# Kernel optimization log

Measured on AMD Instinct MI355X. Metric: run time of the kernel, lower is better.

## Reference

```python
import jax, jax.numpy as jnp
import numpy as np

N = 4096          # n_nodes == batch_size (GFN operates on dense [N,N] adjacency)
E = 65536         # edges per view (avg degree 16)
D = [512, 256, 128]
HV = [128, 64]    # hidden_size_v
HM = [64, 32]     # hidden_size


def _xavier(key, shape):
    fan_in, fan_out = shape[0], shape[1]
    lim = np.sqrt(6.0 / (fan_in + fan_out))
    return jax.random.uniform(key, shape, jnp.float32, -lim, lim)


def setup_inputs() -> dict:
    key = jax.random.key(0)
    ks = jax.random.split(key, 40)
    inp = {}
    inp['data1'] = jax.random.normal(ks[0], (N, D[0]), jnp.float32)
    inp['data2'] = jax.random.normal(ks[1], (N, D[1]), jnp.float32)
    inp['data3'] = jax.random.normal(ks[2], (N, D[2]), jnp.float32)
    # graphs: random edge lists + matching dense adjacency (g.ndata['adj'])
    for v, k_ in zip((1, 2, 3), (ks[3], ks[4], ks[5])):
        ka, kb = jax.random.split(k_)
        src = jax.random.randint(ka, (E,), 0, N, jnp.int32)
        dst = jax.random.randint(kb, (E,), 0, N, jnp.int32)
        adj = np.zeros((N, N), np.float32)
        adj[np.asarray(src), np.asarray(dst)] = 1.0
        inp[f'src{v}'] = src
        inp[f'dst{v}'] = dst
        inp[f'adj{v}'] = jnp.asarray(adj)
    # per-view GraphConv weights (DGL GraphConv: weight [in,out], bias [out])
    dims = {1: [D[0]] + HV, 2: [D[1]] + HV, 3: [D[2]] + HV}
    ki = 6
    for v in (1, 2, 3):
        for l in range(len(HV)):
            inp[f'w{v}_{l}'] = _xavier(ks[ki], (dims[v][l], dims[v][l + 1])); ki += 1
            inp[f'b{v}_{l}'] = jnp.zeros((dims[v][l + 1],), jnp.float32)
    # consensus GraphConv stack
    mdims = [HV[-1]] + HM
    for l in range(len(HM)):
        inp[f'wm_{l}'] = _xavier(ks[ki], (mdims[l], mdims[l + 1])); ki += 1
        inp[f'bm_{l}'] = jnp.zeros((mdims[l + 1],), jnp.float32)
    # FeatureFusion weights [HV[-1], HV[-1]]
    inp['fw1'] = _xavier(ks[ki], (HV[-1], HV[-1])); ki += 1
    inp['fw2'] = _xavier(ks[ki], (HV[-1], HV[-1])); ki += 1
    inp['fw3'] = _xavier(ks[ki], (HV[-1], HV[-1])); ki += 1
    # GFN: Linear(N, N//2) -> ReLU -> Linear(N//2, N); torch Linear weight [out,in]
    H = N // 2
    inp['gfn_w1'] = _xavier(ks[ki], (H, N)); ki += 1
    inp['gfn_b1'] = jnp.zeros((H,), jnp.float32)
    inp['gfn_w2'] = _xavier(ks[ki], (N, H)); ki += 1
    inp['gfn_b2'] = jnp.zeros((N,), jnp.float32)
    return inp


def _gconv(src, dst, x, W, b):
    ones = jnp.ones((src.shape[0],), x.dtype)
    deg_out = jnp.clip(jax.ops.segment_sum(ones, src, num_segments=N), 1.0)
    deg_in = jnp.clip(jax.ops.segment_sum(ones, dst, num_segments=N), 1.0)
    h = (x * jax.lax.rsqrt(deg_out)[:, None]) @ W  # diag norms commute with W
    agg = jax.ops.segment_sum(h[src], dst, num_segments=N)
    return agg * jax.lax.rsqrt(deg_in)[:, None] + b


def _dense_gconv(A, x, W, b):
    # same math on a dense (multigraph-count) adjacency; A[src,dst] counts edges
    deg_out = jnp.clip(A.sum(axis=1), 1.0)
    deg_in = jnp.clip(A.sum(axis=0), 1.0)
    h = (x * jax.lax.rsqrt(deg_out)[:, None]) @ W
    agg = A.T @ h
    return agg * jax.lax.rsqrt(deg_in)[:, None] + b


def reference(data1, data2, data3, src1, dst1, src2, dst2, src3, dst3,
              adj1, adj2, adj3,
              w1_0, b1_0, w1_1, b1_1, w2_0, b2_0, w2_1, b2_1,
              w3_0, b3_0, w3_1, b3_1, wm_0, bm_0, wm_1, bm_1,
              fw1, fw2, fw3, gfn_w1, gfn_b1, gfn_w2, gfn_b2):
    # per-view encoder stacks (relu on all but last layer)
    f1 = jax.nn.relu(_gconv(src1, dst1, data1, w1_0, b1_0))
    f1 = _gconv(src1, dst1, f1, w1_1, b1_1)
    f2 = jax.nn.relu(_gconv(src2, dst2, data2, w2_0, b2_0))
    f2 = _gconv(src2, dst2, f2, w2_1, b2_1)
    f3 = jax.nn.relu(_gconv(src3, dst3, data3, w3_0, b3_0))
    f3 = _gconv(src3, dst3, f3, w3_1, b3_1)
    # FeatureFusion (dropout treated as eval/identity): softmax then relu
    z = f1 @ fw1 + f2 @ fw2 + f3 @ fw3
    z = jax.nn.relu(jax.nn.softmax(z, axis=1))
    # consensus graph: GFN on summed dense adjacency
    adjin = adj1 + adj2 + adj3
    adj_r = jax.nn.relu(adjin @ gfn_w1.T + gfn_b1) @ gfn_w2.T + gfn_b2
    adj_p = jnp.round(jnp.clip(adj_r, 0.0, 1.0) + 0.1)
    # dgl.from_scipy on (adj_p + adj_p.T) keeps edge per nonzero; add_self_loop
    # adds one extra self edge per node -> multigraph edge counts = struct + I
    A = ((adj_p + adj_p.T) != 0).astype(jnp.float32) + jnp.eye(N, dtype=jnp.float32)
    A = jax.lax.stop_gradient(A)  # graph built from detached adj_p
    feat = jax.nn.relu(_dense_gconv(A, z, wm_0, bm_0))
    feat = _dense_gconv(A, feat, wm_1, bm_1)
    # InnerProductDecoder with identity activation (same for every view)
    adj_rec = feat @ feat.T
    return adj_r, adj_rec, feat
```

## Files before the change

kernel.cpp:

```cpp
#include <hip/hip_runtime.h>


#define N_ 4096
#define E_ 65536
#define CSR_STRIDE 73732

typedef __attribute__((ext_vector_type(8))) short short8;
typedef __attribute__((ext_vector_type(4))) float f32x4;

__device__ __forceinline__ float bf2f(unsigned short u) {
  union { unsigned int i; float f; } v; v.i = ((unsigned int)u) << 16; return v.f;
}
__device__ __forceinline__ unsigned short f2bf(float f) {
  union { float f; unsigned int i; } v; v.f = f;
  return (unsigned short)((v.i + 0x7fffu + ((v.i >> 16) & 1u)) >> 16);
}

__global__ void k_edges(const int* __restrict__ s1, const int* __restrict__ d1,
                        const int* __restrict__ s2, const int* __restrict__ d2,
                        const int* __restrict__ s3, const int* __restrict__ d3,
                        float* __restrict__ wd, unsigned* __restrict__ bmp) {
  int v = blockIdx.x >> 8;
  int e = (blockIdx.x & 255) * 256 + threadIdx.x;
  const int* sv = v == 0 ? s1 : (v == 1 ? s2 : s3);
  const int* dv = v == 0 ? d1 : (v == 1 ? d2 : d3);
  int s = sv[e], d = dv[e];
  atomicAdd(&wd[v * 8192 + s], 1.f);
  atomicAdd(&wd[v * 8192 + 4096 + d], 1.f);
  unsigned idx = (unsigned)s * 4096u + (unsigned)d;
  atomicOr(&bmp[v * 524288 + (idx >> 5)], 1u << (idx & 31));
}

__global__ void k_prep(const unsigned* __restrict__ bmp, ushort* __restrict__ adjin,
                       const float4* __restrict__ g1, const float4* __restrict__ g2,
                       ushort* __restrict__ w1h, ushort* __restrict__ w1l,
                       ushort* __restrict__ w2h, ushort* __restrict__ w2l) {
  int i = blockIdx.x * 256 + threadIdx.x;
  if (i < 2097152) {
    int w = i >> 2, sh = (i & 3) << 3;
    unsigned a = bmp[w] >> sh, b = bmp[524288 + w] >> sh, c = bmp[1048576 + w] >> sh;
    short8 o;
#pragma unroll
    for (int k = 0; k < 8; ++k) {
      int cnt = ((a >> k) & 1) + ((b >> k) & 1) + ((c >> k) & 1);
      o[k] = (short)f2bf((float)cnt);
    }
    *(short8*)(adjin + (size_t)i * 8) = o;
  } else {
    int i2 = i - 2097152;
    int hf = i2 >= 2097152;
    int j = i2 & 2097151;
    float4 x = hf ? g2[j] : g1[j];
    ushort* ph = hf ? w2h : w1h;
    ushort* pl = hf ? w2l : w1l;
    ushort4 h, l;
    h.x = f2bf(x.x); l.x = f2bf(x.x - bf2f(h.x));
    h.y = f2bf(x.y); l.y = f2bf(x.y - bf2f(h.y));
    h.z = f2bf(x.z); l.z = f2bf(x.z - bf2f(h.z));
    h.w = f2bf(x.w); l.w = f2bf(x.w - bf2f(h.w));
    *(ushort4*)(ph + (size_t)j * 4) = h;
    *(ushort4*)(pl + (size_t)j * 4) = l;
  }
}

__global__ void k_scan7(float* __restrict__ wd, int* __restrict__ csr) {
  int b = blockIdx.x, t = threadIdx.x;
  if (b < 3) {
    float* di = wd + b * 8192 + 4096;
    int* ptr = csr + b * CSR_STRIDE;
    int* cur = ptr + 4100;
    __shared__ int part[256];
    int local[16];
    float cnt[16];
    int s = 0;
#pragma unroll
    for (int i = 0; i < 16; ++i) { cnt[i] = di[t * 16 + i]; local[i] = s; s += (int)cnt[i]; }
    part[t] = s;
    __syncthreads();
    for (int o = 1; o < 256; o <<= 1) {
      int x = (t >= o) ? part[t - o] : 0;
      __syncthreads();
      part[t] += x;
      __syncthreads();
    }
    int base = (t > 0) ? part[t - 1] : 0;
#pragma unroll
    for (int i = 0; i < 16; ++i) {
      ptr[t * 16 + i] = base + local[i];
      cur[t * 16 + i] = 0;
      di[t * 16 + i] = 1.f / sqrtf(fmaxf(cnt[i], 1.f));
    }
    if (t == 255) ptr[4096] = part[255];
  } else {
    int off = (b == 3) ? 0 : (b == 4) ? 8192 : (b == 5) ? 16384 : 24576;
#pragma unroll
    for (int i = 0; i < 16; ++i) {
      int idx = off + t * 16 + i;
      wd[idx] = 1.f / sqrtf(fmaxf(wd[idx], 1.f));
    }
  }
}

__global__ void k_fill(const int* __restrict__ s1, const int* __restrict__ d1,
                       const int* __restrict__ s2, const int* __restrict__ d2,
                       const int* __restrict__ s3, const int* __restrict__ d3,
                       int* __restrict__ csr) {
  int v = blockIdx.x >> 8;
  int e = (blockIdx.x & 255) * 256 + threadIdx.x;
  const int* sv = v == 0 ? s1 : (v == 1 ? s2 : s3);
  const int* dv = v == 0 ? d1 : (v == 1 ? d2 : d3);
  int* ptr = csr + v * CSR_STRIDE;
  int* cur = ptr + 4100;
  int* cidx = cur + 4096;
  int d = dv[e];
  int pos = ptr[d] + atomicAdd(&cur[d], 1);
  cidx[pos] = sv[e];
}

template<int C, int RELU>
__global__ void k_agg(const float* __restrict__ h, const int* __restrict__ csrv,
                      const float* __restrict__ rs, const float* __restrict__ bias,
                      float* __restrict__ out, int os, int oo) {
  const int* ptr = csrv;
  const int* cidx = csrv + 4100 + 4096;
  int wave = threadIdx.x >> 6, lane = threadIdx.x & 63;
  int dst, col;
  if (C == 128) { dst = (blockIdx.x << 1) + (wave >> 1); col = ((wave & 1) << 6) + lane; }
  else          { dst = (blockIdx.x << 2) + wave;        col = lane; }
  int e0 = ptr[dst], e1 = ptr[dst + 1];
  float acc = 0.f;
  for (int e = e0; e < e1; ++e) acc += h[(size_t)cidx[e] * C + col];
  float v = acc * rs[dst] + bias[col];
  if (RELU) v = fmaxf(v, 0.f);
  out[(size_t)dst * os + oo + col] = v;
}

__global__ void k_softmax(const float* __restrict__ zp, float* __restrict__ z) {
  int row = blockIdx.x * 4 + (threadIdx.x >> 6);
  int lane = threadIdx.x & 63;
  float v = zp[row * 64 + lane];
  float m = v;
  for (int o = 32; o; o >>= 1) m = fmaxf(m, __shfl_xor(m, o, 64));
  float e = expf(v - m);
  float s = e;
  for (int o = 32; o; o >>= 1) s += __shfl_xor(s, o, 64);
  z[row * 64 + lane] = e / s;
}

__global__ void k_buildA(const float* __restrict__ adjr, ushort* __restrict__ Ab,
                         float* __restrict__ degA) {
  int bi = blockIdx.y, bj = blockIdx.x;
  if (bi > bj) return;
  __shared__ float t2[64][65];
  __shared__ ushort at[64][65];
  __shared__ float cs[64];
  int t = threadIdx.x, w = t >> 6, lane = t & 63;
#pragma unroll
  for (int i = 0; i < 16; ++i) {
    int idx = t + i * 256, r = idx >> 6, c = idx & 63;
    t2[r][c] = adjr[(size_t)(bj * 64 + r) * N_ + bi * 64 + c];
  }
  if (t < 64) cs[t] = 0.f;
  __syncthreads();
  float colp = 0.f;
  for (int rr = 0; rr < 16; ++rr) {
    int r = w * 16 + rr;
    int gi = bi * 64 + r, gj = bj * 64 + lane;
    float p1 = rintf(fminf(fmaxf(adjr[(size_t)gi * N_ + gj], 0.f), 1.f) + 0.1f);
    float p2 = rintf(fminf(fmaxf(t2[lane][r], 0.f), 1.f) + 0.1f);
    float a = ((p1 + p2) != 0.f ? 1.f : 0.f) + (gi == gj ? 1.f : 0.f);
    ushort ab = f2bf(a);
    Ab[(size_t)gi * N_ + gj] = ab;
    at[lane][r] = ab;
    colp += a;
    float s = a;
    for (int o = 32; o; o >>= 1) s += __shfl_xor(s, o, 64);
    if (lane == 0) atomicAdd(&degA[gi], s);
  }
  if (bi < bj) {
    atomicAdd(&cs[lane], colp);
    __syncthreads();
#pragma unroll
    for (int i = 0; i < 16; ++i) {
      int idx = t + i * 256, r = idx >> 6, c = idx & 63;
      Ab[(size_t)(bj * 64 + r) * N_ + bi * 64 + c] = at[r][c];
    }
    if (t < 64) atomicAdd(&degA[bj * 64 + t], cs[t]);
  }
}

template<int BN, int TM, int RS>
__global__ __launch_bounds__(256) void k_gemm(
    const float* __restrict__ Ap, int lda, const float* __restrict__ B, int ldb,
    float* __restrict__ C, int ldc, int K, const float* __restrict__ rs) {
  __shared__ float As[64][33];
  __shared__ float Bs[32][BN];
  const int t = threadIdx.x;
  const int bm = blockIdx.x << 6;
  const int bn = blockIdx.y * BN;
  const int cg = t % (BN / 4), rg = t / (BN / 4);
  float av[TM][4];
#pragma unroll
  for (int i = 0; i < TM; ++i)
#pragma unroll
    for (int j = 0; j < 4; ++j) av[i][j] = 0.f;
  for (int k0 = 0; k0 < K; k0 += 32) {
    __syncthreads();
#pragma unroll
    for (int i = 0; i < 8; ++i) {
      int idx = t + (i << 8), r = idx >> 5, c = idx & 31;
      As[r][c] = Ap[(size_t)(bm + r) * lda + k0 + c];
    }
#pragma unroll
    for (int i = 0; i < (BN >> 3); ++i) {
      int idx = t + (i << 8), r = idx / BN, c = idx % BN;
      Bs[r][c] = B[(size_t)(k0 + r) * ldb + bn + c];
    }
    __syncthreads();
#pragma unroll
    for (int k = 0; k < 32; ++k) {
      float b0 = Bs[k][(cg << 2) + 0], b1 = Bs[k][(cg << 2) + 1];
      float b2 = Bs[k][(cg << 2) + 2], b3 = Bs[k][(cg << 2) + 3];
#pragma unroll
      for (int i = 0; i < TM; ++i) {
        float a = As[rg * TM + i][k];
        av[i][0] = fmaf(a, b0, av[i][0]);
        av[i][1] = fmaf(a, b1, av[i][1]);
        av[i][2] = fmaf(a, b2, av[i][2]);
        av[i][3] = fmaf(a, b3, av[i][3]);
      }
    }
  }
#pragma unroll
  for (int i = 0; i < TM; ++i) {
    int gm = bm + rg * TM + i;
    float s = RS ? rs[gm] : 1.f;
#pragma unroll
    for (int j = 0; j < 4; ++j)
      C[(size_t)gm * ldc + bn + (cg << 2) + j] = av[i][j] * s;
  }
}

__global__ __launch_bounds__(256) void k_fuse(
    const float* __restrict__ Ap, const float* __restrict__ F1,
    const float* __restrict__ F2, const float* __restrict__ F3,
    float* __restrict__ C) {
  __shared__ float As[64][33];
  __shared__ float Bs[32][32];
  const int t = threadIdx.x;
  const int bm = blockIdx.x << 6;
  const int bn = blockIdx.y * 32;
  const int cg = t % 8, rg = t / 8;
  float av[2][4];
#pragma unroll
  for (int i = 0; i < 2; ++i)
#pragma unroll
    for (int j = 0; j < 4; ++j) av[i][j] = 0.f;
  for (int k0 = 0; k0 < 192; k0 += 32) {
    __syncthreads();
#pragma unroll
    for (int i = 0; i < 8; ++i) {
      int idx = t + (i << 8), r = idx >> 5, c = idx & 31;
      As[r][c] = Ap[(size_t)(bm + r) * 192 + k0 + c];
    }
#pragma unroll
    for (int i = 0; i < 4; ++i) {
      int idx = t + (i << 8), r = idx >> 5, c = idx & 31;
      int gr = k0 + r;
      const float* Bp = gr < 64 ? F1 : (gr < 128 ? F2 : F3);
      Bs[r][c] = Bp[(gr & 63) * 64 + bn + c];
    }
    __syncthreads();
#pragma unroll
    for (int k = 0; k < 32; ++k) {
      float b0 = Bs[k][(cg << 2) + 0], b1 = Bs[k][(cg << 2) + 1];
      float b2 = Bs[k][(cg << 2) + 2], b3 = Bs[k][(cg << 2) + 3];
#pragma unroll
      for (int i = 0; i < 2; ++i) {
        float a = As[rg * 2 + i][k];
        av[i][0] = fmaf(a, b0, av[i][0]);
        av[i][1] = fmaf(a, b1, av[i][1]);
        av[i][2] = fmaf(a, b2, av[i][2]);
        av[i][3] = fmaf(a, b3, av[i][3]);
      }
    }
  }
#pragma unroll
  for (int i = 0; i < 2; ++i)
#pragma unroll
    for (int j = 0; j < 4; ++j)
      C[(size_t)(bm + rg * 2 + i) * 64 + bn + (cg << 2) + j] = av[i][j];
}

template<int C>
__global__ void k_tsplit(const float* __restrict__ in, ushort* __restrict__ hTh,
                         ushort* __restrict__ hTl) {
  __shared__ float tl[64][C + 1];
  int t = threadIdx.x;
  int m0 = blockIdx.x * 64;
#pragma unroll
  for (int i = 0; i < (C >> 2); ++i) {
    int idx = t + (i << 8), r = idx / C, c = idx % C;
    tl[r][c] = in[(size_t)(m0 + r) * C + c];
  }
  __syncthreads();
#pragma unroll
  for (int i = 0; i < (C >> 2); ++i) {
    int idx = t + (i << 8), c = idx >> 6, mm = idx & 63;
    float v = tl[mm][c];
    ushort hh = f2bf(v);
    hTh[(size_t)c * N_ + m0 + mm] = hh;
    hTl[(size_t)c * N_ + m0 + mm] = f2bf(v - bf2f(hh));
  }
}

template<int BN>
__global__ __launch_bounds__(256) void k_aggm(
    const ushort* __restrict__ Ab, const ushort* __restrict__ hTh,
    const ushort* __restrict__ hTl, float* __restrict__ part) {
  constexpr int NF = BN / 16;
  constexpr int BR = BN / 32;
  __shared__ __align__(16) ushort lA[8192];
  __shared__ __align__(16) ushort lBh[BN * 64];
  __shared__ __align__(16) ushort lBl[BN * 64];
  const int t = threadIdx.x, lane = t & 63, wave = t >> 6;
  const int bm = blockIdx.x << 7;
  const int kb = blockIdx.y << 9;
  const int hi = lane >> 4, r16 = lane & 15, rx = r16 & 7;
  const int srow = t >> 3, sslot = t & 7;

  f32x4 acc[2][NF];
#pragma unroll
  for (int i = 0; i < 2; ++i)
#pragma unroll
    for (int j = 0; j < NF; ++j)
#pragma unroll
      for (int r = 0; r < 4; ++r) acc[i][j][r] = 0.f;

  short8 sA[4], sBh[BR], sBl[BR];
#define ALOAD(KT)                                                                     \
  {                                                                                   \
    _Pragma("unroll") for (int i = 0; i < 4; ++i) {                                   \
      int row = (i << 5) + srow;                                                      \
      sA[i] = *(const short8*)(Ab + (size_t)(bm + row) * 4096 + kb + (KT) + (sslot << 3)); \
    }                                                                                 \
    _Pragma("unroll") for (int i = 0; i < BR; ++i) {                                  \
      int row = (i << 5) + srow;                                                      \
      sBh[i] = *(const short8*)(hTh + (size_t)row * 4096 + kb + (KT) + (sslot << 3)); \
      sBl[i] = *(const short8*)(hTl + (size_t)row * 4096 + kb + (KT) + (sslot << 3)); \
    }                                                                                 \
  }
  ALOAD(0);
  for (int kt = 0; kt < 512; kt += 64) {
    __syncthreads();
#pragma unroll
    for (int i = 0; i < 4; ++i) {
      int row = (i << 5) + srow;
      *(short8*)(&lA[row * 64 + ((sslot ^ (row & 7)) << 3)]) = sA[i];
    }
#pragma unroll
    for (int i = 0; i < BR; ++i) {
      int row = (i << 5) + srow;
      *(short8*)(&lBh[row * 64 + ((sslot ^ (row & 7)) << 3)]) = sBh[i];
      *(short8*)(&lBl[row * 64 + ((sslot ^ (row & 7)) << 3)]) = sBl[i];
    }
    __syncthreads();
    if (kt + 64 < 512) ALOAD(kt + 64);
#pragma unroll
    for (int k0 = 0; k0 < 2; ++k0) {
      const int soff = (((k0 << 2) + hi) ^ rx) << 3;
      short8 af[2], bh[NF], bl[NF];
#pragma unroll
      for (int mi = 0; mi < 2; ++mi) {
        int row = wave * 32 + mi * 16 + r16;
        af[mi] = *(const short8*)(&lA[row * 64 + soff]);
      }
#pragma unroll
      for (int ni = 0; ni < NF; ++ni) {
        int row = ni * 16 + r16;
        bh[ni] = *(const short8*)(&lBh[row * 64 + soff]);
        bl[ni] = *(const short8*)(&lBl[row * 64 + soff]);
      }
#pragma unroll
      for (int mi = 0; mi < 2; ++mi)
#pragma unroll
        for (int ni = 0; ni < NF; ++ni) {
          acc[mi][ni] = __builtin_amdgcn_mfma_f32_16x16x32_bf16(af[mi], bh[ni], acc[mi][ni], 0, 0, 0);
          acc[mi][ni] = __builtin_amdgcn_mfma_f32_16x16x32_bf16(af[mi], bl[ni], acc[mi][ni], 0, 0, 0);
        }
    }
  }
#pragma unroll
  for (int mi = 0; mi < 2; ++mi)
#pragma unroll
    for (int ni = 0; ni < NF; ++ni)
#pragma unroll
      for (int r2 = 0; r2 < 4; ++r2) {
        int gm = bm + wave * 32 + mi * 16 + (hi << 2) + r2;
        int gn = ni * 16 + r16;
        part[((size_t)blockIdx.y * 4096 + gm) * BN + gn] = acc[mi][ni][r2];
      }
#undef ALOAD
}

template<int C, int RELU, int WFT>
__global__ void k_fincons(const float* __restrict__ part, const float* __restrict__ rs,
                          const float* __restrict__ bias, float* __restrict__ out,
                          float* __restrict__ featT) {
  int i = blockIdx.x * 256 + threadIdx.x;
  int m = i / C, c = i % C;
  float s = 0.f;
#pragma unroll
  for (int z = 0; z < 8; ++z) s += part[((size_t)z * 4096 + m) * C + c];
  float v = s * rs[m] + bias[c];
  if (RELU) v = fmaxf(v, 0.f);
  out[i] = v;
  if (WFT) featT[(size_t)c * N_ + m] = v;
}

template<int NA, int NB, int EPI>
__global__ __launch_bounds__(256, 2) void k_mfma(
    const ushort* __restrict__ A0, const ushort* __restrict__ A1,
    const ushort* __restrict__ B0, const ushort* __restrict__ B1,
    const float* __restrict__ bias, float* __restrict__ Cf,
    ushort* __restrict__ Oh, ushort* __restrict__ Ol, int Nn, int K) {
  constexpr int NOPS = NA + NB;
  __shared__ __align__(16) ushort lds[NOPS * 8192];
  const int t = threadIdx.x, lane = t & 63;
  const int wave = t >> 6, wm = wave >> 1, wn = wave & 1;
  const int bm = blockIdx.y << 7, bn = blockIdx.x << 7;
  const int hi = lane >> 4, r16 = lane & 15, rx = r16 & 7;
  const int srow = t >> 3, sslot = t & 7;

  const ushort* gsrc[4];
  int rb[4];
  {
    int no = 0;
    gsrc[no] = A0; rb[no] = bm; no++;
    if (NA > 1) { gsrc[no] = A1; rb[no] = bm; no++; }
    gsrc[no] = B0; rb[no] = bn; no++;
    if (NB > 1) { gsrc[no] = B1; rb[no] = bn; no++; }
  }

  f32x4 acc[4][4];
#pragma unroll
  for (int i = 0; i < 4; ++i)
#pragma unroll
    for (int j = 0; j < 4; ++j)
#pragma unroll
      for (int r = 0; r < 4; ++r) acc[i][j][r] = 0.f;

  short8 stg[NOPS][4];
#define LOADT(KT)                                                                      \
  {                                                                                    \
    _Pragma("unroll") for (int op = 0; op < NOPS; ++op)                                \
        _Pragma("unroll") for (int i = 0; i < 4; ++i) {                                \
      int row = (i << 5) + srow;                                                       \
      stg[op][i] = *(const short8*)(gsrc[op] + (size_t)(rb[op] + row) * K + (KT) +     \
                                    (sslot << 3));                                     \
    }                                                                                  \
  }

  LOADT(0);
  for (int kt = 0; kt < K; kt += 64) {
    __syncthreads();
#pragma unroll
    for (int op = 0; op < NOPS; ++op)
#pragma unroll
      for (int i = 0; i < 4; ++i) {
        int row = (i << 5) + srow;
        *(short8*)(&lds[op * 8192 + row * 64 + ((sslot ^ (row & 7)) << 3)]) = stg[op][i];
      }
    __syncthreads();
    if (kt + 64 < K) LOADT(kt + 64);
#pragma unroll
    for (int k0 = 0; k0 < 2; ++k0) {
      const int soff = (((k0 << 2) + hi) ^ rx) << 3;
      short8 af[NA][4], bf[NB][4];
#pragma unroll
      for (int mi = 0; mi < 4; ++mi) {
        int row = (wm << 6) + (mi << 4) + r16;
        af[0][mi] = *(const short8*)(&lds[row * 64 + soff]);
        if (NA > 1) af[1][mi] = *(const short8*)(&lds[8192 + row * 64 + soff]);
      }
#pragma unroll
      for (int ni = 0; ni < 4; ++ni) {
        int row = (wn << 6) + (ni << 4) + r16;
        bf[0][ni] = *(const short8*)(&lds[NA * 8192 + row * 64 + soff]);
        if (NB > 1) bf[1][ni] = *(const short8*)(&lds[(NA + 1) * 8192 + row * 64 + soff]);
      }
#pragma unroll
      for (int mi = 0; mi < 4; ++mi)
#pragma unroll
        for (int ni = 0; ni < 4; ++ni) {
          acc[mi][ni] = __builtin_amdgcn_mfma_f32_16x16x32_bf16(af[0][mi], bf[0][ni], acc[mi][ni], 0, 0, 0);
          if (NB > 1)
            acc[mi][ni] = __builtin_amdgcn_mfma_f32_16x16x32_bf16(af[0][mi], bf[1][ni], acc[mi][ni], 0, 0, 0);
          if (NA > 1)
            acc[mi][ni] = __builtin_amdgcn_mfma_f32_16x16x32_bf16(af[1][mi], bf[0][ni], acc[mi][ni], 0, 0, 0);
        }
    }
  }
#pragma unroll
  for (int mi = 0; mi < 4; ++mi)
#pragma unroll
    for (int ni = 0; ni < 4; ++ni) {
      const int gn = bn + (wn << 6) + (ni << 4) + r16;
      const float bv = bias[gn];
#pragma unroll
      for (int r2 = 0; r2 < 4; ++r2) {
        const int gm = bm + (wm << 6) + (mi << 4) + (hi << 2) + r2;
        float v = acc[mi][ni][r2] + bv;
        if (EPI == 1) {
          v = fmaxf(v, 0.f);
          ushort hh = f2bf(v);
          Oh[(size_t)gm * Nn + gn] = hh;
          Ol[(size_t)gm * Nn + gn] = f2bf(v - bf2f(hh));
        } else {
          Cf[(size_t)gm * Nn + gn] = v;
        }
      }
    }
#undef LOADT
}

extern "C" void kernel_launch(void* const* d_in, const int* in_sizes, int n_in,
                              void* d_out, int out_size, void* d_ws, size_t ws_size,
                              hipStream_t stream) {
  const float* data[3] = {(const float*)d_in[0], (const float*)d_in[1], (const float*)d_in[2]};
  const int D[3] = {512, 256, 128};
  const int* src[3] = {(const int*)d_in[3], (const int*)d_in[6], (const int*)d_in[9]};
  const int* dst[3] = {(const int*)d_in[4], (const int*)d_in[7], (const int*)d_in[10]};
  const float* w0[3] = {(const float*)d_in[12], (const float*)d_in[16], (const float*)d_in[20]};
  const float* b0[3] = {(const float*)d_in[13], (const float*)d_in[17], (const float*)d_in[21]};
  const float* w1[3] = {(const float*)d_in[14], (const float*)d_in[18], (const float*)d_in[22]};
  const float* b1[3] = {(const float*)d_in[15], (const float*)d_in[19], (const float*)d_in[23]};
  const float* wm0 = (const float*)d_in[24];
  const float* bm0 = (const float*)d_in[25];
  const float* wm1 = (const float*)d_in[26];
  const float* bm1 = (const float*)d_in[27];
  const float* fw[3] = {(const float*)d_in[28], (const float*)d_in[29], (const float*)d_in[30]};
  const float* gw1 = (const float*)d_in[31];
  const float* gb1 = (const float*)d_in[32];
  const float* gw2 = (const float*)d_in[33];
  const float* gb2 = (const float*)d_in[34];

  float* outf = (float*)d_out;
  float* adj_r = outf;
  float* adj_rec = outf + 16777216;
  float* feat = outf + 33554432;
  ushort* w1h = (ushort*)outf;
  ushort* w1l = w1h + 8388608;
  ushort* adjin = w1h + 16777216;
  ushort* o1u = (ushort*)adj_rec;
  ushort* h1h = o1u;
  ushort* h1l = o1u + 8388608;
  ushort* w2h = o1u + 16777216;
  ushort* w2l = o1u + 25165824;
  ushort* Ab = o1u;

  float* wsf = (float*)d_ws;
  float* degA = wsf + 24576;
  unsigned* bmp = (unsigned*)(wsf + 28672);
  float* hX = wsf + 28672;
  float* hbuf = wsf + 552960;
  float* t2 = wsf + 1077248;
  float* fvI = wsf + 1339392;
  int* csr = (int*)(wsf + 2125824);
  float* zpre = wsf + 28672;
  float* zb = wsf + 290816;
  float* part0 = wsf + 552960;
  float* t0 = wsf + 28672;
  ushort* hT0h = (ushort*)(wsf + 290816);
  ushort* hT0l = hT0h + 262144;
  float* h1c = wsf + 28672;
  float* t1 = wsf + 290816;
  ushort* hT1h = (ushort*)(wsf + 421888);
  ushort* hT1l = hT1h + 131072;
  float* part1 = wsf + 552960;
  float* featT = wsf + 28672;

  hipMemsetAsync(wsf, 0, (size_t)1601536 * 4, stream);
  k_edges<<<768, 256, 0, stream>>>(src[0], dst[0], src[1], dst[1], src[2], dst[2], wsf, bmp);
  k_prep<<<24576, 256, 0, stream>>>(bmp, adjin, (const float4*)gw1, (const float4*)gw2,
                                    w1h, w1l, w2h, w2l);
  k_mfma<1, 2, 1><<<dim3(16, 32), 256, 0, stream>>>(
      adjin, nullptr, w1h, w1l, gb1, nullptr, h1h, h1l, 2048, 4096);
  k_mfma<2, 2, 2><<<dim3(32, 32), 256, 0, stream>>>(
      h1h, h1l, w2h, w2l, gb2, adj_r, nullptr, nullptr, 4096, 2048);
  k_buildA<<<dim3(64, 64), 256, 0, stream>>>(adj_r, Ab, degA);

  k_scan7<<<7, 256, 0, stream>>>(wsf, csr);
  k_fill<<<768, 256, 0, stream>>>(src[0], dst[0], src[1], dst[1], src[2], dst[2], csr);
  for (int v = 0; v < 3; ++v) {
    const float* rso = wsf + v * 8192;
    const float* rsi = wsf + v * 8192 + 4096;
    const int* csrv = csr + v * CSR_STRIDE;
    k_gemm<32, 2, 1><<<dim3(64, 4), 256, 0, stream>>>(
        data[v], D[v], w0[v], 128, hX, 128, D[v], rso);
    k_agg<128, 1><<<2048, 256, 0, stream>>>(hX, csrv, rsi, b0[v], hbuf, 128, 0);
    k_gemm<32, 2, 1><<<dim3(64, 2), 256, 0, stream>>>(
        hbuf, 128, w1[v], 64, t2, 64, 128, rso);
    k_agg<64, 0><<<1024, 256, 0, stream>>>(t2, csrv, rsi, b1[v], fvI, 192, v * 64);
  }
  k_fuse<<<dim3(64, 2), 256, 0, stream>>>(fvI, fw[0], fw[1], fw[2], zpre);
  k_softmax<<<1024, 256, 0, stream>>>(zpre, zb);

  k_gemm<32, 2, 1><<<dim3(64, 2), 256, 0, stream>>>(zb, 64, wm0, 64, t0, 64, 64, degA);
  k_tsplit<64><<<64, 256, 0, stream>>>(t0, hT0h, hT0l);
  k_aggm<64><<<dim3(32, 8), 256, 0, stream>>>(Ab, hT0h, hT0l, part0);
  k_fincons<64, 1, 0><<<1024, 256, 0, stream>>>(part0, degA, bm0, h1c, nullptr);
  k_gemm<32, 2, 1><<<dim3(64, 1), 256, 0, stream>>>(h1c, 64, wm1, 32, t1, 32, 64, degA);
  k_tsplit<32><<<64, 256, 0, stream>>>(t1, hT1h, hT1l);
  k_aggm<32><<<dim3(32, 8), 256, 0, stream>>>(Ab, hT1h, hT1l, part1);
  k_fincons<32, 0, 1><<<512, 256, 0, stream>>>(part1, degA, bm1, feat, featT);
  k_gemm<128, 8, 0><<<dim3(64, 32), 256, 0, stream>>>(
      feat, 32, featT, 4096, adj_rec, 4096, 32, nullptr);
}
```

Before: 952.1 us.

## Move small GEMMs and decoder to split-bf16 MFMA, batch views, bitpack adjacency

Replaces the scalar FP32 tiled GEMMs with a split-bf16 (hi/lo) MFMA GEMM that handles all three views in one launch, and pre-converts all small weights in a single prep kernel. The adj_r epilogue now emits a ballot-packed bitmask of the rounded adjacency, so buildA reads bits instead of re-reading the dense float matrix. The per-view aggregation loops are merged into single 3-view launches with vectorized loads. The feat·featT decoder becomes a dedicated MFMA kernel. Together these cut launches, dense-matrix traffic and FP32 ALU work, at the cost of bf16x3 split precision and more complex buffer aliasing in the output scratch.

```diff
diff --git a/kernel.cpp b/kernel.cpp
--- a/kernel.cpp
+++ b/kernel.cpp
@@ -63,6 +63,21 @@
   }
 }
 
+struct WSeg { const float* src; ushort* dh; ushort* dl; int Kw; int Nw; int sh; int os; int oo; };
+struct WArgs { WSeg s[11]; };
+
+__global__ void k_wprep(WArgs wa) {
+  WSeg sg = wa.s[blockIdx.y];
+  int total = sg.Kw << sg.sh;
+  for (int i = blockIdx.x * 256 + threadIdx.x; i < total; i += 8192) {
+    int k = i >> sg.sh, n = i & (sg.Nw - 1);
+    float v = sg.src[i];
+    ushort hh = f2bf(v);
+    sg.dh[(size_t)n * sg.os + sg.oo + k] = hh;
+    sg.dl[(size_t)n * sg.os + sg.oo + k] = f2bf(v - bf2f(hh));
+  }
+}
+
 __global__ void k_scan7(float* __restrict__ wd, int* __restrict__ csr) {
   int b = blockIdx.x, t = threadIdx.x;
   if (b < 3) {
@@ -117,22 +132,40 @@
   cidx[pos] = sv[e];
 }
 
+struct AB { const float* b[3]; };
 template<int C, int RELU>
-__global__ void k_agg(const float* __restrict__ h, const int* __restrict__ csrv,
-                      const float* __restrict__ rs, const float* __restrict__ bias,
-                      float* __restrict__ out, int os, int oo) {
-  const int* ptr = csrv;
-  const int* cidx = csrv + 4100 + 4096;
+__global__ void k_agg3(const float* __restrict__ hbase, int is,
+                       const int* __restrict__ csr, const float* __restrict__ wd,
+                       AB ab, float* __restrict__ out, int os) {
+  int v = blockIdx.y;
+  const int* ptr = csr + v * CSR_STRIDE;
+  const int* cidx = ptr + 4100 + 4096;
+  const float* rs = wd + v * 8192 + 4096;
+  const float* bias = ab.b[v];
+  const float* hv = hbase + v * C;
+  float* ov = out + v * C;
   int wave = threadIdx.x >> 6, lane = threadIdx.x & 63;
-  int dst, col;
-  if (C == 128) { dst = (blockIdx.x << 1) + (wave >> 1); col = ((wave & 1) << 6) + lane; }
-  else          { dst = (blockIdx.x << 2) + wave;        col = lane; }
+  int dst = (blockIdx.x << 2) + wave;
   int e0 = ptr[dst], e1 = ptr[dst + 1];
-  float acc = 0.f;
-  for (int e = e0; e < e1; ++e) acc += h[(size_t)cidx[e] * C + col];
-  float v = acc * rs[dst] + bias[col];
-  if (RELU) v = fmaxf(v, 0.f);
-  out[(size_t)dst * os + oo + col] = v;
+  float sc = rs[dst];
+  if (C == 128) {
+    float2 acc = {0.f, 0.f};
+    for (int e = e0; e < e1; ++e) {
+      float2 x = *(const float2*)(hv + (size_t)cidx[e] * is + lane * 2);
+      acc.x += x.x; acc.y += x.y;
+    }
+    float2 r;
+    r.x = acc.x * sc + bias[lane * 2];
+    r.y = acc.y * sc + bias[lane * 2 + 1];
+    if (RELU) { r.x = fmaxf(r.x, 0.f); r.y = fmaxf(r.y, 0.f); }
+    *(float2*)(ov + (size_t)dst * os + lane * 2) = r;
+  } else {
+    float acc = 0.f;
+    for (int e = e0; e < e1; ++e) acc += hv[(size_t)cidx[e] * is + lane];
+    float r = acc * sc + bias[lane];
+    if (RELU) r = fmaxf(r, 0.f);
+    ov[(size_t)dst * os + lane] = r;
+  }
 }
 
 __global__ void k_softmax(const float* __restrict__ zp, float* __restrict__ z) {
@@ -147,149 +180,131 @@
   z[row * 64 + lane] = e / s;
 }
 
-__global__ void k_buildA(const float* __restrict__ adjr, ushort* __restrict__ Ab,
-                         float* __restrict__ degA) {
+__global__ void k_buildA2(const ushort* __restrict__ pb, ushort* __restrict__ Ab,
+                          float* __restrict__ degA) {
   int bi = blockIdx.y, bj = blockIdx.x;
-  if (bi > bj) return;
-  __shared__ float t2[64][65];
-  __shared__ ushort at[64][65];
-  __shared__ float cs[64];
   int t = threadIdx.x, w = t >> 6, lane = t & 63;
-#pragma unroll
-  for (int i = 0; i < 16; ++i) {
-    int idx = t + i * 256, r = idx >> 6, c = idx & 63;
-    t2[r][c] = adjr[(size_t)(bj * 64 + r) * N_ + bi * 64 + c];
-  }
-  if (t < 64) cs[t] = 0.f;
-  __syncthreads();
-  float colp = 0.f;
+  int gj = bj * 64 + lane;
+  unsigned long long tp = *(const unsigned long long*)(pb + (size_t)gj * 256 + bi * 4);
   for (int rr = 0; rr < 16; ++rr) {
     int r = w * 16 + rr;
-    int gi = bi * 64 + r, gj = bj * 64 + lane;
-    float p1 = rintf(fminf(fmaxf(adjr[(size_t)gi * N_ + gj], 0.f), 1.f) + 0.1f);
-    float p2 = rintf(fminf(fmaxf(t2[lane][r], 0.f), 1.f) + 0.1f);
-    float a = ((p1 + p2) != 0.f ? 1.f : 0.f) + (gi == gj ? 1.f : 0.f);
-    ushort ab = f2bf(a);
-    Ab[(size_t)gi * N_ + gj] = ab;
-    at[lane][r] = ab;
-    colp += a;
+    int gi = bi * 64 + r;
+    unsigned long long prow = *(const unsigned long long*)(pb + (size_t)gi * 256 + bj * 4);
+    int pbit = (int)((prow >> lane) & 1ull);
+    int tbit = (int)((tp >> r) & 1ull);
+    float a = ((pbit | tbit) ? 1.f : 0.f) + (gi == gj ? 1.f : 0.f);
+    Ab[(size_t)gi * N_ + gj] = f2bf(a);
     float s = a;
     for (int o = 32; o; o >>= 1) s += __shfl_xor(s, o, 64);
     if (lane == 0) atomicAdd(&degA[gi], s);
   }
-  if (bi < bj) {
-    atomicAdd(&cs[lane], colp);
+}
+
+struct GSeg { const float* A; const ushort* bh; const ushort* bl; float* C;
+              const float* rs; int lda; int ldc; int K; };
+struct GArgs { GSeg s[3]; };
+
+template<int BN, int NSEG>
+__global__ __launch_bounds__(256) void k_gemms(GArgs ga) {
+  constexpr int NF = BN / 16;
+  constexpr int BR = BN / 32;
+  __shared__ __align__(16) ushort lAh[8192], lAl[8192];
+  __shared__ __align__(16) ushort lBh[BN * 64], lBl[BN * 64];
+  const GSeg sg = ga.s[NSEG == 1 ? 0 : blockIdx.y];
+  const int t = threadIdx.x, lane = t & 63, wave = t >> 6;
+  const int bm = blockIdx.x << 7;
+  const int hi = lane >> 4, r16 = lane & 15, rx = r16 & 7;
+  const int srow = t >> 3, sslot = t & 7;
+
+  f32x4 acc[2][NF];
+#pragma unroll
+  for (int i = 0; i < 2; ++i)
+#pragma unroll
+    for (int j = 0; j < NF; ++j)
+#pragma unroll
+      for (int r = 0; r < 4; ++r) acc[i][j][r] = 0.f;
+
+  float4 sa[4][2];
+  short8 sbh[BR], sbl[BR];
+#define GLOAD(KT)                                                                     \
+  {                                                                                   \
+    _Pragma("unroll") for (int i = 0; i < 4; ++i) {                                   \
+      int row = (i << 5) + srow;                                                      \
+      const float* ap = sg.A + (size_t)(bm + row) * sg.lda + (KT) + (sslot << 3);     \
+      sa[i][0] = *(const float4*)ap;                                                  \
+      sa[i][1] = *(const float4*)(ap + 4);                                            \
+    }                                                                                 \
+    _Pragma("unroll") for (int i = 0; i < BR; ++i) {                                  \
+      int row = (i << 5) + srow;                                                      \
+      sbh[i] = *(const short8*)(sg.bh + (size_t)row * sg.K + (KT) + (sslot << 3));    \
+      sbl[i] = *(const short8*)(sg.bl + (size_t)row * sg.K + (KT) + (sslot << 3));    \
+    }                                                                                 \
+  }
+  GLOAD(0);
+  for (int kt = 0; kt < sg.K; kt += 64) {
     __syncthreads();
 #pragma unroll
-    for (int i = 0; i < 16; ++i) {
-      int idx = t + i * 256, r = idx >> 6, c = idx & 63;
-      Ab[(size_t)(bj * 64 + r) * N_ + bi * 64 + c] = at[r][c];
-    }
-    if (t < 64) atomicAdd(&degA[bj * 64 + t], cs[t]);
-  }
-}
-
-template<int BN, int TM, int RS>
-__global__ __launch_bounds__(256) void k_gemm(
-    const float* __restrict__ Ap, int lda, const float* __restrict__ B, int ldb,
-    float* __restrict__ C, int ldc, int K, const float* __restrict__ rs) {
-  __shared__ float As[64][33];
-  __shared__ float Bs[32][BN];
-  const int t = threadIdx.x;
-  const int bm = blockIdx.x << 6;
-  const int bn = blockIdx.y * BN;
-  const int cg = t % (BN / 4), rg = t / (BN / 4);
-  float av[TM][4];
-#pragma unroll
-  for (int i = 0; i < TM; ++i)
-#pragma unroll
-    for (int j = 0; j < 4; ++j) av[i][j] = 0.f;
-  for (int k0 = 0; k0 < K; k0 += 32) {
+    for (int i = 0; i < 4; ++i) {
+      int row = (i << 5) + srow;
+      short8 h8, l8;
+      const float* fp = (const float*)&sa[i][0];
+#pragma unroll
+      for (int j = 0; j < 8; ++j) {
+        float f = fp[j];
+        ushort hh = f2bf(f);
+        h8[j] = (short)hh;
+        l8[j] = (short)f2bf(f - bf2f(hh));
+      }
+      int so = row * 64 + ((sslot ^ (row & 7)) << 3);
+      *(short8*)(&lAh[so]) = h8;
+      *(short8*)(&lAl[so]) = l8;
+    }
+#pragma unroll
+    for (int i = 0; i < BR; ++i) {
+      int row = (i << 5) + srow;
+      int so = row * 64 + ((sslot ^ (row & 7)) << 3);
+      *(short8*)(&lBh[so]) = sbh[i];
+      *(short8*)(&lBl[so]) = sbl[i];
+    }
     __syncthreads();
-#pragma unroll
-    for (int i = 0; i < 8; ++i) {
-      int idx = t + (i << 8), r = idx >> 5, c = idx & 31;
-      As[r][c] = Ap[(size_t)(bm + r) * lda + k0 + c];
-    }
-#pragma unroll
-    for (int i = 0; i < (BN >> 3); ++i) {
-      int idx = t + (i << 8), r = idx / BN, c = idx % BN;
-      Bs[r][c] = B[(size_t)(k0 + r) * ldb + bn + c];
-    }
-    __syncthreads();
-#pragma unroll
-    for (int k = 0; k < 32; ++k) {
-      float b0 = Bs[k][(cg << 2) + 0], b1 = Bs[k][(cg << 2) + 1];
-      float b2 = Bs[k][(cg << 2) + 2], b3 = Bs[k][(cg << 2) + 3];
-#pragma unroll
-      for (int i = 0; i < TM; ++i) {
-        float a = As[rg * TM + i][k];
-        av[i][0] = fmaf(a, b0, av[i][0]);
-        av[i][1] = fmaf(a, b1, av[i][1]);
-        av[i][2] = fmaf(a, b2, av[i][2]);
-        av[i][3] = fmaf(a, b3, av[i][3]);
-      }
-    }
-  }
-#pragma unroll
-  for (int i = 0; i < TM; ++i) {
-    int gm = bm + rg * TM + i;
-    float s = RS ? rs[gm] : 1.f;
-#pragma unroll
-    for (int j = 0; j < 4; ++j)
-      C[(size_t)gm * ldc + bn + (cg << 2) + j] = av[i][j] * s;
-  }
-}
-
-__global__ __launch_bounds__(256) void k_fuse(
-    const float* __restrict__ Ap, const float* __restrict__ F1,
-    const float* __restrict__ F2, const float* __restrict__ F3,
-    float* __restrict__ C) {
-  __shared__ float As[64][33];
-  __shared__ float Bs[32][32];
-  const int t = threadIdx.x;
-  const int bm = blockIdx.x << 6;
-  const int bn = blockIdx.y * 32;
-  const int cg = t % 8, rg = t / 8;
-  float av[2][4];
-#pragma unroll
-  for (int i = 0; i < 2; ++i)
-#pragma unroll
-    for (int j = 0; j < 4; ++j) av[i][j] = 0.f;
-  for (int k0 = 0; k0 < 192; k0 += 32) {
-    __syncthreads();
-#pragma unroll
-    for (int i = 0; i < 8; ++i) {
-      int idx = t + (i << 8), r = idx >> 5, c = idx & 31;
-      As[r][c] = Ap[(size_t)(bm + r) * 192 + k0 + c];
-    }
-#pragma unroll
-    for (int i = 0; i < 4; ++i) {
-      int idx = t + (i << 8), r = idx >> 5, c = idx & 31;
-      int gr = k0 + r;
-      const float* Bp = gr < 64 ? F1 : (gr < 128 ? F2 : F3);
-      Bs[r][c] = Bp[(gr & 63) * 64 + bn + c];
-    }
-    __syncthreads();
-#pragma unroll
-    for (int k = 0; k < 32; ++k) {
-      float b0 = Bs[k][(cg << 2) + 0], b1 = Bs[k][(cg << 2) + 1];
-      float b2 = Bs[k][(cg << 2) + 2], b3 = Bs[k][(cg << 2) + 3];
-#pragma unroll
-      for (int i = 0; i < 2; ++i) {
-        float a = As[rg * 2 + i][k];
-        av[i][0] = fmaf(a, b0, av[i][0]);
-        av[i][1] = fmaf(a, b1, av[i][1]);
-        av[i][2] = fmaf(a, b2, av[i][2]);
-        av[i][3] = fmaf(a, b3, av[i][3]);
-      }
-    }
-  }
-#pragma unroll
-  for (int i = 0; i < 2; ++i)
-#pragma unroll
-    for (int j = 0; j < 4; ++j)
-      C[(size_t)(bm + rg * 2 + i) * 64 + bn + (cg << 2) + j] = av[i][j];
+    if (kt + 64 < sg.K) GLOAD(kt + 64);
+#pragma unroll
+    for (int k0 = 0; k0 < 2; ++k0) {
+      const int soff = (((k0 << 2) + hi) ^ rx) << 3;
+      short8 ah_[2], al_[2];
+#pragma unroll
+      for (int mi = 0; mi < 2; ++mi) {
+        int row = wave * 32 + mi * 16 + r16;
+        ah_[mi] = *(const short8*)(&lAh[row * 64 + soff]);
+        al_[mi] = *(const short8*)(&lAl[row * 64 + soff]);
+      }
+#pragma unroll
+      for (int nf = 0; nf < NF; ++nf) {
+        int row = nf * 16 + r16;
+        short8 bh_ = *(const short8*)(&lBh[row * 64 + soff]);
+        short8 bl_ = *(const short8*)(&lBl[row * 64 + soff]);
+#pragma unroll
+        for (int mi = 0; mi < 2; ++mi) {
+          acc[mi][nf] = __builtin_amdgcn_mfma_f32_16x16x32_bf16(ah_[mi], bh_, acc[mi][nf], 0, 0, 0);
+          acc[mi][nf] = __builtin_amdgcn_mfma_f32_16x16x32_bf16(ah_[mi], bl_, acc[mi][nf], 0, 0, 0);
+          acc[mi][nf] = __builtin_amdgcn_mfma_f32_16x16x32_bf16(al_[mi], bh_, acc[mi][nf], 0, 0, 0);
+        }
+      }
+    }
+  }
+#pragma unroll
+  for (int mi = 0; mi < 2; ++mi)
+#pragma unroll
+    for (int nf = 0; nf < NF; ++nf)
+#pragma unroll
+      for (int r2 = 0; r2 < 4; ++r2) {
+        int gm = bm + wave * 32 + mi * 16 + (hi << 2) + r2;
+        int gn = nf * 16 + r16;
+        float v = acc[mi][nf][r2];
+        if (sg.rs) v *= sg.rs[gm];
+        sg.C[(size_t)gm * sg.ldc + gn] = v;
+      }
+#undef GLOAD
 }
 
 template<int C>
@@ -406,7 +421,7 @@
 template<int C, int RELU, int WFT>
 __global__ void k_fincons(const float* __restrict__ part, const float* __restrict__ rs,
                           const float* __restrict__ bias, float* __restrict__ out,
-                          float* __restrict__ featT) {
+                          ushort* __restrict__ fh, ushort* __restrict__ fl) {
   int i = blockIdx.x * 256 + threadIdx.x;
   int m = i / C, c = i % C;
   float s = 0.f;
@@ -415,7 +430,50 @@
   float v = s * rs[m] + bias[c];
   if (RELU) v = fmaxf(v, 0.f);
   out[i] = v;
-  if (WFT) featT[(size_t)c * N_ + m] = v;
+  if (WFT) {
+    ushort hh = f2bf(v);
+    fh[i] = hh;
+    fl[i] = f2bf(v - bf2f(hh));
+  }
+}
+
+__global__ __launch_bounds__(256) void k_rec(const ushort* __restrict__ fh,
+                                             const ushort* __restrict__ fl,
+                                             float* __restrict__ out) {
+  const int t = threadIdx.x, lane = t & 63;
+  const int wave = t >> 6, wm = wave >> 1, wn = wave & 1;
+  const int bm = blockIdx.y << 7, bn = blockIdx.x << 7;
+  const int hi = lane >> 4, r16 = lane & 15;
+  short8 ah[4], al[4], bh[4], bl[4];
+#pragma unroll
+  for (int mi = 0; mi < 4; ++mi) {
+    int row = bm + (wm << 6) + (mi << 4) + r16;
+    ah[mi] = *(const short8*)(fh + (size_t)row * 32 + (hi << 3));
+    al[mi] = *(const short8*)(fl + (size_t)row * 32 + (hi << 3));
+  }
+#pragma unroll
+  for (int ni = 0; ni < 4; ++ni) {
+    int row = bn + (wn << 6) + (ni << 4) + r16;
+    bh[ni] = *(const short8*)(fh + (size_t)row * 32 + (hi << 3));
+    bl[ni] = *(const short8*)(fl + (size_t)row * 32 + (hi << 3));
+  }
+#pragma unroll
+  for (int mi = 0; mi < 4; ++mi)
+#pragma unroll
+    for (int ni = 0; ni < 4; ++ni) {
+      f32x4 acc;
+#pragma unroll
+      for (int r = 0; r < 4; ++r) acc[r] = 0.f;
+      acc = __builtin_amdgcn_mfma_f32_16x16x32_bf16(ah[mi], bh[ni], acc, 0, 0, 0);
+      acc = __builtin_amdgcn_mfma_f32_16x16x32_bf16(ah[mi], bl[ni], acc, 0, 0, 0);
+      acc = __builtin_amdgcn_mfma_f32_16x16x32_bf16(al[mi], bh[ni], acc, 0, 0, 0);
+#pragma unroll
+      for (int r2 = 0; r2 < 4; ++r2) {
+        int gm = bm + (wm << 6) + (mi << 4) + (hi << 2) + r2;
+        int gn = bn + (wn << 6) + (ni << 4) + r16;
+        out[(size_t)gm * N_ + gn] = acc[r2];
+      }
+    }
 }
 
 template<int NA, int NB, int EPI>
@@ -423,7 +481,8 @@
     const ushort* __restrict__ A0, const ushort* __restrict__ A1,
     const ushort* __restrict__ B0, const ushort* __restrict__ B1,
     const float* __restrict__ bias, float* __restrict__ Cf,
-    ushort* __restrict__ Oh, ushort* __restrict__ Ol, int Nn, int K) {
+    ushort* __restrict__ Oh, ushort* __restrict__ Ol, int Nn, int K,
+    ushort* __restrict__ Pb) {
   constexpr int NOPS = NA + NB;
   __shared__ __align__(16) ushort lds[NOPS * 8192];
   const int t = threadIdx.x, lane = t & 63;
@@ -518,6 +577,10 @@
           Ol[(size_t)gm * Nn + gn] = f2bf(v - bf2f(hh));
         } else {
           Cf[(size_t)gm * Nn + gn] = v;
+          float p = rintf(fminf(fmaxf(v, 0.f), 1.f) + 0.1f);
+          unsigned long long mask = __ballot(p != 0.f);
+          if (r16 == 0)
+            Pb[(size_t)gm * 256 + (gn >> 4)] = (ushort)(mask >> (hi << 4));
         }
       }
     }
@@ -558,62 +621,103 @@
   ushort* w2h = o1u + 16777216;
   ushort* w2l = o1u + 25165824;
   ushort* Ab = o1u;
+  float* SCR = outf + 25165824;
+  float* hbuf3 = SCR;
+  float* t2c = SCR + 1572864;
+  float* part = SCR + 2359296;
 
   float* wsf = (float*)d_ws;
   float* degA = wsf + 24576;
   unsigned* bmp = (unsigned*)(wsf + 28672);
-  float* hX = wsf + 28672;
-  float* hbuf = wsf + 552960;
-  float* t2 = wsf + 1077248;
-  float* fvI = wsf + 1339392;
+  ushort* pb = (ushort*)(wsf + 28672);
+  float* hX3 = wsf + 28672;
+  float* fvI = wsf + 28672;
+  float* zpre = wsf + 815104;
+  float* zb = wsf + 1077248;
+  float* t0 = wsf + 1339392;
+  ushort* hT0h = (ushort*)(wsf + 28672);
+  ushort* hT0l = (ushort*)(wsf + 159744);
+  float* h1c = wsf + 290816;
+  float* t1 = wsf + 552960;
+  ushort* hT1h = (ushort*)(wsf + 28672);
+  ushort* hT1l = (ushort*)(wsf + 94208);
+  ushort* fh = (ushort*)(wsf + 159744);
+  ushort* fl = (ushort*)(wsf + 225280);
   int* csr = (int*)(wsf + 2125824);
-  float* zpre = wsf + 28672;
-  float* zb = wsf + 290816;
-  float* part0 = wsf + 552960;
-  float* t0 = wsf + 28672;
-  ushort* hT0h = (ushort*)(wsf + 290816);
-  ushort* hT0l = hT0h + 262144;
-  float* h1c = wsf + 28672;
-  float* t1 = wsf + 290816;
-  ushort* hT1h = (ushort*)(wsf + 421888);
-  ushort* hT1l = hT1h + 131072;
-  float* part1 = wsf + 552960;
-  float* featT = wsf + 28672;
+  ushort* WT = (ushort*)(wsf + 2347264);
+
+  const int o_w0h[3] = {0, 131072, 196608}, o_w0l[3] = {65536, 163840, 212992};
+  const int o_w1h[3] = {229376, 245760, 262144}, o_w1l[3] = {237568, 253952, 270336};
+  const int o_fwh = 278528, o_fwl = 290816;
+  const int o_m0h = 303104, o_m0l = 307200, o_m1h = 311296, o_m1l = 313344;
 
   hipMemsetAsync(wsf, 0, (size_t)1601536 * 4, stream);
   k_edges<<<768, 256, 0, stream>>>(src[0], dst[0], src[1], dst[1], src[2], dst[2], wsf, bmp);
   k_prep<<<24576, 256, 0, stream>>>(bmp, adjin, (const float4*)gw1, (const float4*)gw2,
                                     w1h, w1l, w2h, w2l);
+  {
+    WArgs wa;
+    for (int v = 0; v < 3; ++v) {
+      wa.s[v] = {w0[v], WT + o_w0h[v], WT + o_w0l[v], D[v], 128, 7, D[v], 0};
+      wa.s[3 + v] = {w1[v], WT + o_w1h[v], WT + o_w1l[v], 128, 64, 6, 128, 0};
+      wa.s[6 + v] = {fw[v], WT + o_fwh, WT + o_fwl, 64, 64, 6, 192, v * 64};
+    }
+    wa.s[9] = {wm0, WT + o_m0h, WT + o_m0l, 64, 64, 6, 64, 0};
+    wa.s[10] = {wm1, WT + o_m1h, WT + o_m1l, 64, 32, 5, 64, 0};
+    k_wprep<<<dim3(32, 11), 256, 0, stream>>>(wa);
+  }
   k_mfma<1, 2, 1><<<dim3(16, 32), 256, 0, stream>>>(
-      adjin, nullptr, w1h, w1l, gb1, nullptr, h1h, h1l, 2048, 4096);
+      adjin, nullptr, w1h, w1l, gb1, nullptr, h1h, h1l, 2048, 4096, nullptr);
   k_mfma<2, 2, 2><<<dim3(32, 32), 256, 0, stream>>>(
-      h1h, h1l, w2h, w2l, gb2, adj_r, nullptr, nullptr, 4096, 2048);
-  k_buildA<<<dim3(64, 64), 256, 0, stream>>>(adj_r, Ab, degA);
+      h1h, h1l, w2h, w2l, gb2, adj_r, nullptr, nullptr, 4096, 2048, pb);
+  k_buildA2<<<dim3(64, 64), 256, 0, stream>>>(pb, Ab, degA);
 
   k_scan7<<<7, 256, 0, stream>>>(wsf, csr);
   k_fill<<<768, 256, 0, stream>>>(src[0], dst[0], src[1], dst[1], src[2], dst[2], csr);
-  for (int v = 0; v < 3; ++v) {
-    const float* rso = wsf + v * 8192;
-    const float* rsi = wsf + v * 8192 + 4096;
-    const int* csrv = csr + v * CSR_STRIDE;
-    k_gemm<32, 2, 1><<<dim3(64, 4), 256, 0, stream>>>(
-        data[v], D[v], w0[v], 128, hX, 128, D[v], rso);
-    k_agg<128, 1><<<2048, 256, 0, stream>>>(hX, csrv, rsi, b0[v], hbuf, 128, 0);
-    k_gemm<32, 2, 1><<<dim3(64, 2), 256, 0, stream>>>(
-        hbuf, 128, w1[v], 64, t2, 64, 128, rso);
-    k_agg<64, 0><<<1024, 256, 0, stream>>>(t2, csrv, rsi, b1[v], fvI, 192, v * 64);
-  }
-  k_fuse<<<dim3(64, 2), 256, 0, stream>>>(fvI, fw[0], fw[1], fw[2], zpre);
+  {
+    GArgs g0;
+    for (int v = 0; v < 3; ++v)
+      g0.s[v] = {data[v], WT + o_w0h[v], WT + o_w0l[v], hX3 + v * 128,
+                 wsf + v * 8192, D[v], 384, D[v]};
+    k_gemms<128, 3><<<dim3(32, 3), 256, 0, stream>>>(g0);
+  }
+  {
+    AB ab = {{b0[0], b0[1], b0[2]}};
+    k_agg3<128, 1><<<dim3(1024, 3), 256, 0, stream>>>(hX3, 384, csr, wsf, ab, hbuf3, 384);
+  }
+  {
+    GArgs g1;
+    for (int v = 0; v < 3; ++v)
+      g1.s[v] = {hbuf3 + v * 128, WT + o_w1h[v], WT + o_w1l[v], t2c + v * 64,
+                 wsf + v * 8192, 384, 192, 128};
+    k_gemms<64, 3><<<dim3(32, 3), 256, 0, stream>>>(g1);
+  }
+  {
+    AB ab = {{b1[0], b1[1], b1[2]}};
+    k_agg3<64, 0><<<dim3(1024, 3), 256, 0, stream>>>(t2c, 192, csr, wsf, ab, fvI, 192);
+  }
+  {
+    GArgs gf;
+    gf.s[0] = {fvI, WT + o_fwh, WT + o_fwl, zpre, nullptr, 192, 64, 192};
+    k_gemms<64, 1><<<dim3(32, 1), 256, 0, stream>>>(gf);
+  }
   k_softmax<<<1024, 256, 0, stream>>>(zpre, zb);
 
-  k_gemm<32, 2, 1><<<dim3(64, 2), 256, 0, stream>>>(zb, 64, wm0, 64, t0, 64, 64, degA);
+  {
+    GArgs gm;
+    gm.s[0] = {zb, WT + o_m0h, WT + o_m0l, t0, degA, 64, 64, 64};
+    k_gemms<64, 1><<<dim3(32, 1), 256, 0, stream>>>(gm);
+  }
   k_tsplit<64><<<64, 256, 0, stream>>>(t0, hT0h, hT0l);
-  k_aggm<64><<<dim3(32, 8), 256, 0, stream>>>(Ab, hT0h, hT0l, part0);
-  k_fincons<64, 1, 0><<<1024, 256, 0, stream>>>(part0, degA, bm0, h1c, nullptr);
-  k_gemm<32, 2, 1><<<dim3(64, 1), 256, 0, stream>>>(h1c, 64, wm1, 32, t1, 32, 64, degA);
+  k_aggm<64><<<dim3(32, 8), 256, 0, stream>>>(Ab, hT0h, hT0l, part);
+  k_fincons<64, 1, 0><<<1024, 256, 0, stream>>>(part, degA, bm0, h1c, nullptr, nullptr);
+  {
+    GArgs gm;
+    gm.s[0] = {h1c, WT + o_m1h, WT + o_m1l, t1, degA, 64, 32, 64};
+    k_gemms<32, 1><<<dim3(32, 1), 256, 0, stream>>>(gm);
+  }
   k_tsplit<32><<<64, 256, 0, stream>>>(t1, hT1h, hT1l);
-  k_aggm<32><<<dim3(32, 8), 256, 0, stream>>>(Ab, hT1h, hT1l, part1);
-  k_fincons<32, 0, 1><<<512, 256, 0, stream>>>(part1, degA, bm1, feat, featT);
-  k_gemm<128, 8, 0><<<dim3(64, 32), 256, 0, stream>>>(
-      feat, 32, featT, 4096, adj_rec, 4096, 32, nullptr);
-}
+  k_aggm<32><<<dim3(32, 8), 256, 0, stream>>>(Ab, hT1h, hT1l, part);
+  k_fincons<32, 0, 1><<<512, 256, 0, stream>>>(part, degA, bm1, feat, fh, fl);
+  k_rec<<<dim3(32, 32), 256, 0, stream>>>(fh, fl, adj_rec);
+}
```

Result: faster. 894.1 us (-6.1%).
